# Kernel optimization log

Measured on AMD Instinct MI355X. Metric: run time of the kernel, lower is better.

## Reference

```python
import jax, jax.numpy as jnp
import numpy as np

N, E, IN_F, OUT_F, HEADS = 50000, 800000, 256, 64, 8


def setup_inputs() -> dict:
    key = jax.random.key(0)
    k1, k2, k3, k4, k5 = jax.random.split(key, 5)
    stdv = 1.0 / np.sqrt(OUT_F)
    return {
        "h": jax.random.normal(k1, (N, IN_F), dtype=jnp.float32),
        "weight": jax.random.uniform(k2, (IN_F, OUT_F), minval=-stdv, maxval=stdv, dtype=jnp.float32),
        "attention_w": jax.random.normal(k3, (1, HEADS), dtype=jnp.float32),
        "src": jax.random.randint(k4, (E,), 0, N, dtype=jnp.int32),
        "dst": jax.random.randint(k5, (E,), 0, N, dtype=jnp.int32),
    }


def reference(h, weight, attention_w, src, dst):
    n_nodes = h.shape[0]
    hp = h @ weight                              # [N, F] projected features
    hs = hp[src]                                 # [E, F] gather source feats
    hd = hp[dst]                                 # [E, F] gather dest feats
    dot = jnp.sum(hs * hd, axis=-1, keepdims=True)   # [E, 1] edge dot attention
    # original: (msg[:, F, 1] @ attention_w[1, H]).sum(H) == msg * attention_w.sum()
    msg = dot * hs * jnp.sum(attention_w)        # [E, F]
    accum = jax.ops.segment_sum(msg, dst, num_segments=n_nodes)  # [N, F]
    # DGL update_all: zero in-degree nodes keep their projected feature
    deg = jax.ops.segment_sum(jnp.ones((src.shape[0], 1), hp.dtype), dst, num_segments=n_nodes)
    return jnp.where(deg > 0, accum, hp)
```

## Files before the change

kernel.cpp:

```cpp
#include <hip/hip_runtime.h>

#define IN_F 256
#define OUT_F 64
#define NBKT_MAX 1024
#define PART_BLOCKS 128
#define HIST_BLOCKS 256

typedef __attribute__((ext_vector_type(8))) short short8;
typedef __attribute__((ext_vector_type(4))) float f32x4;
typedef unsigned int uint32;

#define AS_I(f) __builtin_bit_cast(int, f)
#define AS_F(i) __builtin_bit_cast(float, i)
#define DPP_ADD(v, ctrl, rmask) \
    v += AS_F(__builtin_amdgcn_update_dpp(0, AS_I(v), ctrl, rmask, 0xf, true))

__device__ __forceinline__ float half_sum_sel(float p, bool hi) {
    DPP_ADD(p, 0x111, 0xf);
    DPP_ADD(p, 0x112, 0xf);
    DPP_ADD(p, 0x114, 0xf);
    DPP_ADD(p, 0x118, 0xf);
    DPP_ADD(p, 0x142, 0xa);
    float dlo = AS_F(__builtin_amdgcn_readlane(AS_I(p), 31));
    float dhi = AS_F(__builtin_amdgcn_readlane(AS_I(p), 63));
    return hi ? dhi : dlo;
}

__device__ __forceinline__ unsigned short f2bf(float f) {
    uint32 u = __builtin_bit_cast(uint32, f);
    u += 0x7fffu + ((u >> 16) & 1u);
    return (unsigned short)(u >> 16);
}
__device__ __forceinline__ float bf2f(unsigned short s) {
    return __builtin_bit_cast(float, (uint32)s << 16);
}

__global__ __launch_bounds__(256) void gemm_hist_kernel(const float* __restrict__ h,
                                                        const float* __restrict__ w,
                                                        unsigned short* __restrict__ hpb,
                                                        int N,
                                                        const int* __restrict__ dst,
                                                        int* __restrict__ bkt_cnt,
                                                        int E, int NB, int ngemm) {
    __shared__ char smem[32768];
    int b = blockIdx.x, t = threadIdx.x;

    if (b >= ngemm) {
        int* lcnt = (int*)smem;
        int hb = b - ngemm;
        for (int i = t; i < NB; i += 256) lcnt[i] = 0;
        __syncthreads();
        for (int e = hb * 256 + t; e < E; e += HIST_BLOCKS * 256)
            atomicAdd(&lcnt[dst[e] >> 6], 1);
        __syncthreads();
        for (int i = t; i < NB; i += 256)
            if (lcnt[i]) atomicAdd(&bkt_cnt[i], lcnt[i]);
        return;
    }

    short8* wfrag = (short8*)smem;
    for (int slot = t; slot < 2048; slot += 256) {
        int kb = slot >> 6, n = slot & 63;
        short8 v;
#pragma unroll
        for (int jj = 0; jj < 8; ++jj)
            v[jj] = (short)f2bf(w[(size_t)(kb * 8 + jj) * OUT_F + n]);
        wfrag[slot] = v;
    }
    __syncthreads();

    int wave = t >> 6, lane = t & 63;
    int n16  = lane & 15, quad = lane >> 4;
    int base = b * 64 + wave * 16;
    int arow_i = base + n16; if (arow_i >= N) arow_i = N - 1;
    const float* arow = h + (size_t)arow_i * IN_F;

    f32x4 acc[4];
#pragma unroll
    for (int ct = 0; ct < 4; ++ct) acc[ct] = (f32x4){0.f, 0.f, 0.f, 0.f};

#pragma unroll
    for (int ks = 0; ks < 8; ++ks) {
        int k0 = ks * 32;
        float4 a0 = *(const float4*)(arow + k0 + quad * 8);
        float4 a1 = *(const float4*)(arow + k0 + quad * 8 + 4);
        short8 af;
        af[0] = (short)f2bf(a0.x); af[1] = (short)f2bf(a0.y);
        af[2] = (short)f2bf(a0.z); af[3] = (short)f2bf(a0.w);
        af[4] = (short)f2bf(a1.x); af[5] = (short)f2bf(a1.y);
        af[6] = (short)f2bf(a1.z); af[7] = (short)f2bf(a1.w);
        int kb = ks * 4 + quad;
#pragma unroll
        for (int ct = 0; ct < 4; ++ct) {
            short8 bf = wfrag[kb * 64 + ct * 16 + n16];
            acc[ct] = __builtin_amdgcn_mfma_f32_16x16x32_bf16(af, bf, acc[ct], 0, 0, 0);
        }
    }

#pragma unroll
    for (int ct = 0; ct < 4; ++ct) {
#pragma unroll
        for (int r = 0; r < 4; ++r) {
            int ro = base + quad * 4 + r;
            if (ro < N) hpb[(size_t)ro * OUT_F + ct * 16 + n16] = f2bf(acc[ct][r]);
        }
    }
}

__global__ __launch_bounds__(256) void partition_kernel(const int* __restrict__ src,
                                                        const int* __restrict__ dst,
                                                        const int* __restrict__ bkt_cnt,
                                                        int* __restrict__ bkt_cursor,
                                                        int* __restrict__ bkt_base,
                                                        uint32* __restrict__ pairs,
                                                        int E, int NB) {
    __shared__ int sbase[NBKT_MAX + 1];
    __shared__ int lcnt[NBKT_MAX];
    __shared__ int gbase[NBKT_MAX];
    __shared__ int wsum2[4];

    int t = threadIdx.x, lane = t & 63, wid = t >> 6;

    int loc[4];
    int s = 0;
#pragma unroll
    for (int j = 0; j < 4; ++j) {
        int idx = t * 4 + j;
        int x = (idx < NB) ? bkt_cnt[idx] : 0;
        loc[j] = s; s += x;
    }
    int xs = s;
#pragma unroll
    for (int off = 1; off < 64; off <<= 1) {
        int y = __shfl_up(xs, off, 64);
        if (lane >= off) xs += y;
    }
    if (lane == 63) wsum2[wid] = xs;
    __syncthreads();
    int base_w = 0;
    for (int k = 0; k < wid; ++k) base_w += wsum2[k];
    int toff = base_w + xs - s;
#pragma unroll
    for (int j = 0; j < 4; ++j) {
        int idx = t * 4 + j;
        if (idx < NB) sbase[idx] = toff + loc[j];
    }
    if (t == 0) sbase[NB] = E;
    __syncthreads();

    if (blockIdx.x == 0) {
        for (int i = t; i <= NB; i += 256) bkt_base[i] = sbase[i];
    }

    int chunk = (E + PART_BLOCKS - 1) / PART_BLOCKS;
    int s0 = blockIdx.x * chunk;
    int s1 = min(E, s0 + chunk);

    for (int i = t; i < NB; i += 256) lcnt[i] = 0;
    __syncthreads();
    for (int e = s0 + t; e < s1; e += 256)
        atomicAdd(&lcnt[dst[e] >> 6], 1);
    __syncthreads();
    for (int i = t; i < NB; i += 256) {
        int c = lcnt[i];
        if (c) gbase[i] = sbase[i] + atomicAdd(&bkt_cursor[i], c);
        lcnt[i] = 0;
    }
    __syncthreads();
    for (int e = s0 + t; e < s1; e += 256) {
        int d  = dst[e];
        int bk = d >> 6;
        int idx = atomicAdd(&lcnt[bk], 1);
        pairs[gbase[bk] + idx] = (uint32)src[e] | ((uint32)(d & 63) << 26);
    }
}

__global__ __launch_bounds__(256) void sortlocal_kernel(const uint32* __restrict__ pairs,
                                                        const int* __restrict__ bkt_base,
                                                        int* __restrict__ srcs,
                                                        int* __restrict__ row_ptr,
                                                        int N, int E) {
    __shared__ int bin[64], excl[65], cur[64];
    int b = blockIdx.x, t = threadIdx.x;
    int beg = bkt_base[b], end = bkt_base[b + 1];

    if (t < 64) bin[t] = 0;
    __syncthreads();
    for (int i = beg + t; i < end; i += 256)
        atomicAdd(&bin[pairs[i] >> 26], 1);
    __syncthreads();
    if (t < 64) {
        int v = bin[t], x = v;
#pragma unroll
        for (int off = 1; off < 64; off <<= 1) {
            int y = __shfl_up(x, off, 64);
            if (t >= off) x += y;
        }
        excl[t] = x - v;
        cur[t]  = x - v;
        if (t == 63) excl[64] = x;
    }
    __syncthreads();
    if (t < 65) {
        int idx = b * 64 + t;
        if (idx <= N) row_ptr[idx] = beg + excl[t];
    }
    for (int i = beg + t; i < end; i += 256) {
        uint32 p = pairs[i];
        int dl   = (int)(p >> 26);
        int pos  = atomicAdd(&cur[dl], 1);
        srcs[beg + pos] = (int)(p & 0x3FFFFFFu);
    }
}

#define GATH(S) (*(const uint32*)(hpb + (size_t)(S) * OUT_F + half * 2))
#define PROC(Q) { float a0 = bf2f((unsigned short)((Q) & 0xffff));            \
                  float a1 = bf2f((unsigned short)((Q) >> 16));               \
                  float dd = half_sum_sel(fmaf(a1, hd1, a0 * hd0), hi);       \
                  acc0 = fmaf(dd, a0, acc0); acc1 = fmaf(dd, a1, acc1); }

__global__ __launch_bounds__(256) void accum_kernel(const unsigned short* __restrict__ hpb,
                                                    const int* __restrict__ row_ptr,
                                                    const int* __restrict__ srcs,
                                                    const float* __restrict__ attw,
                                                    float* __restrict__ out, int N) {
    int v    = (blockIdx.x * blockDim.x + threadIdx.x) >> 6;
    int lane = threadIdx.x & 63;
    if (v >= N) return;

    int  half = lane & 31;
    bool hi   = lane >= 32;

    int beg = row_ptr[v];
    int end = row_ptr[v + 1];

    uint32 hd2 = *(const uint32*)(hpb + (size_t)v * OUT_F + half * 2);
    float hd0 = bf2f((unsigned short)(hd2 & 0xffff));
    float hd1 = bf2f((unsigned short)(hd2 >> 16));

    float c = 0.f;
#pragma unroll
    for (int i = 0; i < 8; ++i) c += attw[i];

    float acc0 = 0.f, acc1 = 0.f;
    int j = beg;

    for (; j + 32 <= end; j += 32) {
        const int4* sp = (const int4*)(srcs + j);
        int4 sa = sp[0], sb = sp[1], sc = sp[2], sd = sp[3];
        int4 se = sp[4], sf = sp[5], sg = sp[6], sh = sp[7];
        uint32 q0  = GATH(hi ? sa.y : sa.x), q1  = GATH(hi ? sa.w : sa.z);
        uint32 q2  = GATH(hi ? sb.y : sb.x), q3  = GATH(hi ? sb.w : sb.z);
        uint32 q4  = GATH(hi ? sc.y : sc.x), q5  = GATH(hi ? sc.w : sc.z);
        uint32 q6  = GATH(hi ? sd.y : sd.x), q7  = GATH(hi ? sd.w : sd.z);
        uint32 q8  = GATH(hi ? se.y : se.x), q9  = GATH(hi ? se.w : se.z);
        uint32 q10 = GATH(hi ? sf.y : sf.x), q11 = GATH(hi ? sf.w : sf.z);
        uint32 q12 = GATH(hi ? sg.y : sg.x), q13 = GATH(hi ? sg.w : sg.z);
        uint32 q14 = GATH(hi ? sh.y : sh.x), q15 = GATH(hi ? sh.w : sh.z);
        PROC(q0)  PROC(q1)  PROC(q2)  PROC(q3)
        PROC(q4)  PROC(q5)  PROC(q6)  PROC(q7)
        PROC(q8)  PROC(q9)  PROC(q10) PROC(q11)
        PROC(q12) PROC(q13) PROC(q14) PROC(q15)
    }
    for (; j + 8 <= end; j += 8) {
        const int4* sp = (const int4*)(srcs + j);
        int4 sa = sp[0], sb = sp[1];
        uint32 q0 = GATH(hi ? sa.y : sa.x), q1 = GATH(hi ? sa.w : sa.z);
        uint32 q2 = GATH(hi ? sb.y : sb.x), q3 = GATH(hi ? sb.w : sb.z);
        PROC(q0) PROC(q1) PROC(q2) PROC(q3)
    }
    for (; j + 2 <= end; j += 2) {
        int s_lo = srcs[j], s_hi = srcs[j + 1];
        uint32 q = GATH(hi ? s_hi : s_lo);
        PROC(q)
    }
    if (j < end) {
        uint32 q = GATH(srcs[j]);
        float a0 = bf2f((unsigned short)(q & 0xffff));
        float a1 = bf2f((unsigned short)(q >> 16));
        float dd = half_sum_sel(fmaf(a1, hd1, a0 * hd0), false);
        if (!hi) {
            acc0 = fmaf(dd, a0, acc0);
            acc1 = fmaf(dd, a1, acc1);
        }
    }

    acc0 += __shfl_xor(acc0, 32, 64);
    acc1 += __shfl_xor(acc1, 32, 64);

    if (!hi) {
        float r0, r1;
        if (end > beg) { r0 = acc0 * c; r1 = acc1 * c; }
        else           { r0 = hd0;      r1 = hd1;      }
        *(float2*)(out + (size_t)v * OUT_F + half * 2) = make_float2(r0, r1);
    }
}

extern "C" void kernel_launch(void* const* d_in, const int* in_sizes, int n_in,
                              void* d_out, int out_size, void* d_ws, size_t ws_size,
                              hipStream_t stream) {
    const float* h    = (const float*)d_in[0];
    const float* w    = (const float*)d_in[1];
    const float* attw = (const float*)d_in[2];
    const int*   src  = (const int*)d_in[3];
    const int*   dst  = (const int*)d_in[4];

    int N = in_sizes[0] / IN_F;
    int E = in_sizes[3];
    int NB = (N + 63) >> 6;
    int ngemm = (N + 63) / 64;

    float* out = (float*)d_out;

    char* p = (char*)d_ws;
    unsigned short* hpb = (unsigned short*)p;  p += (size_t)N * OUT_F * sizeof(unsigned short);
    int* bkt_cnt    = (int*)p;                 p += (NBKT_MAX + 1) * sizeof(int);
    int* bkt_cursor = (int*)p;                 p += (NBKT_MAX + 1) * sizeof(int);
    int* bkt_base   = (int*)p;                 p += (NBKT_MAX + 1) * sizeof(int);
    int* row_ptr    = (int*)p;                 p += ((size_t)N + 8) * sizeof(int);
    uint32* pairs   = (uint32*)p;              p += (size_t)E * sizeof(uint32);
    int* srcs       = (int*)p;

    hipMemsetAsync(bkt_cnt, 0, 2 * (NBKT_MAX + 1) * sizeof(int), stream);

    gemm_hist_kernel<<<ngemm + HIST_BLOCKS, 256, 0, stream>>>(h, w, hpb, N,
                                                              dst, bkt_cnt, E, NB, ngemm);

    partition_kernel<<<PART_BLOCKS, 256, 0, stream>>>(src, dst, bkt_cnt, bkt_cursor,
                                                      bkt_base, pairs, E, NB);

    sortlocal_kernel<<<NB, 256, 0, stream>>>(pairs, bkt_base, srcs, row_ptr, N, E);

    accum_kernel<<<((size_t)N * 64 + 255) / 256, 256, 0, stream>>>(hpb, row_ptr, srcs, attw, out, N);
}
```

Measured before the change: 172.5 us.

## Fuse bucket-local sort into accumulation kernel using LDS-resident source lists

Removes the separate sortlocal kernel and its srcs/row_ptr global arrays. Each 512-thread block now sorts its 64-node bucket's pairs into shared memory and then aggregates all 64 nodes from LDS, with 8 waves each handling 8 nodes. This saves one kernel launch and a global write/read round trip of the edge list. Buckets larger than CAP fall back to a slow linear scan. The partition kernel moves to 512 threads, and the accumulation inner unroll shrinks from 32 to 16 edges.

```diff
diff --git a/kernel.cpp b/kernel.cpp
--- a/kernel.cpp
+++ b/kernel.cpp
@@ -5,6 +5,7 @@
 #define NBKT_MAX 1024
 #define PART_BLOCKS 128
 #define HIST_BLOCKS 256
+#define CAP 3072
 
 typedef __attribute__((ext_vector_type(8))) short short8;
 typedef __attribute__((ext_vector_type(4))) float f32x4;
@@ -107,7 +108,7 @@
     }
 }
 
-__global__ __launch_bounds__(256) void partition_kernel(const int* __restrict__ src,
+__global__ __launch_bounds__(512) void partition_kernel(const int* __restrict__ src,
                                                         const int* __restrict__ dst,
                                                         const int* __restrict__ bkt_cnt,
                                                         int* __restrict__ bkt_cursor,
@@ -117,18 +118,15 @@
     __shared__ int sbase[NBKT_MAX + 1];
     __shared__ int lcnt[NBKT_MAX];
     __shared__ int gbase[NBKT_MAX];
-    __shared__ int wsum2[4];
+    __shared__ int wsum2[8];
 
     int t = threadIdx.x, lane = t & 63, wid = t >> 6;
 
-    int loc[4];
-    int s = 0;
-#pragma unroll
-    for (int j = 0; j < 4; ++j) {
-        int idx = t * 4 + j;
-        int x = (idx < NB) ? bkt_cnt[idx] : 0;
-        loc[j] = s; s += x;
-    }
+    int loc0, loc1;
+    int x0 = (t * 2     < NB) ? bkt_cnt[t * 2]     : 0;
+    int x1 = (t * 2 + 1 < NB) ? bkt_cnt[t * 2 + 1] : 0;
+    loc0 = 0; loc1 = x0;
+    int s = x0 + x1;
     int xs = s;
 #pragma unroll
     for (int off = 1; off < 64; off <<= 1) {
@@ -140,76 +138,35 @@
     int base_w = 0;
     for (int k = 0; k < wid; ++k) base_w += wsum2[k];
     int toff = base_w + xs - s;
-#pragma unroll
-    for (int j = 0; j < 4; ++j) {
-        int idx = t * 4 + j;
-        if (idx < NB) sbase[idx] = toff + loc[j];
-    }
+    if (t * 2     < NB) sbase[t * 2]     = toff + loc0;
+    if (t * 2 + 1 < NB) sbase[t * 2 + 1] = toff + loc1;
     if (t == 0) sbase[NB] = E;
     __syncthreads();
 
     if (blockIdx.x == 0) {
-        for (int i = t; i <= NB; i += 256) bkt_base[i] = sbase[i];
+        for (int i = t; i <= NB; i += 512) bkt_base[i] = sbase[i];
     }
 
     int chunk = (E + PART_BLOCKS - 1) / PART_BLOCKS;
     int s0 = blockIdx.x * chunk;
     int s1 = min(E, s0 + chunk);
 
-    for (int i = t; i < NB; i += 256) lcnt[i] = 0;
-    __syncthreads();
-    for (int e = s0 + t; e < s1; e += 256)
+    for (int i = t; i < NB; i += 512) lcnt[i] = 0;
+    __syncthreads();
+    for (int e = s0 + t; e < s1; e += 512)
         atomicAdd(&lcnt[dst[e] >> 6], 1);
     __syncthreads();
-    for (int i = t; i < NB; i += 256) {
+    for (int i = t; i < NB; i += 512) {
         int c = lcnt[i];
         if (c) gbase[i] = sbase[i] + atomicAdd(&bkt_cursor[i], c);
         lcnt[i] = 0;
     }
     __syncthreads();
-    for (int e = s0 + t; e < s1; e += 256) {
+    for (int e = s0 + t; e < s1; e += 512) {
         int d  = dst[e];
         int bk = d >> 6;
         int idx = atomicAdd(&lcnt[bk], 1);
         pairs[gbase[bk] + idx] = (uint32)src[e] | ((uint32)(d & 63) << 26);
-    }
-}
-
-__global__ __launch_bounds__(256) void sortlocal_kernel(const uint32* __restrict__ pairs,
-                                                        const int* __restrict__ bkt_base,
-                                                        int* __restrict__ srcs,
-                                                        int* __restrict__ row_ptr,
-                                                        int N, int E) {
-    __shared__ int bin[64], excl[65], cur[64];
-    int b = blockIdx.x, t = threadIdx.x;
-    int beg = bkt_base[b], end = bkt_base[b + 1];
-
-    if (t < 64) bin[t] = 0;
-    __syncthreads();
-    for (int i = beg + t; i < end; i += 256)
-        atomicAdd(&bin[pairs[i] >> 26], 1);
-    __syncthreads();
-    if (t < 64) {
-        int v = bin[t], x = v;
-#pragma unroll
-        for (int off = 1; off < 64; off <<= 1) {
-            int y = __shfl_up(x, off, 64);
-            if (t >= off) x += y;
-        }
-        excl[t] = x - v;
-        cur[t]  = x - v;
-        if (t == 63) excl[64] = x;
-    }
-    __syncthreads();
-    if (t < 65) {
-        int idx = b * 64 + t;
-        if (idx <= N) row_ptr[idx] = beg + excl[t];
-    }
-    for (int i = beg + t; i < end; i += 256) {
-        uint32 p = pairs[i];
-        int dl   = (int)(p >> 26);
-        int pos  = atomicAdd(&cur[dl], 1);
-        srcs[beg + pos] = (int)(p & 0x3FFFFFFu);
     }
 }
 
@@ -219,80 +176,148 @@
                   float dd = half_sum_sel(fmaf(a1, hd1, a0 * hd0), hi);       \
                   acc0 = fmaf(dd, a0, acc0); acc1 = fmaf(dd, a1, acc1); }
 
-__global__ __launch_bounds__(256) void accum_kernel(const unsigned short* __restrict__ hpb,
-                                                    const int* __restrict__ row_ptr,
-                                                    const int* __restrict__ srcs,
-                                                    const float* __restrict__ attw,
-                                                    float* __restrict__ out, int N) {
-    int v    = (blockIdx.x * blockDim.x + threadIdx.x) >> 6;
-    int lane = threadIdx.x & 63;
-    if (v >= N) return;
-
-    int  half = lane & 31;
-    bool hi   = lane >= 32;
-
-    int beg = row_ptr[v];
-    int end = row_ptr[v + 1];
-
-    uint32 hd2 = *(const uint32*)(hpb + (size_t)v * OUT_F + half * 2);
-    float hd0 = bf2f((unsigned short)(hd2 & 0xffff));
-    float hd1 = bf2f((unsigned short)(hd2 >> 16));
+__global__ __launch_bounds__(512) void accum_sort_kernel(const unsigned short* __restrict__ hpb,
+                                                         const uint32* __restrict__ pairs,
+                                                         const int* __restrict__ bkt_base,
+                                                         const float* __restrict__ attw,
+                                                         float* __restrict__ out, int N) {
+    __shared__ int slds[CAP];
+    __shared__ int bin[64], excl[65], cur[64];
+
+    int b = blockIdx.x, t = threadIdx.x;
+    int wid = t >> 6, lane = t & 63;
+    int half = lane & 31;
+    bool hi  = lane >= 32;
+    int node0 = b * 64;
+
+    int beg = bkt_base[b], end = bkt_base[b + 1];
+    int nE  = end - beg;
 
     float c = 0.f;
 #pragma unroll
     for (int i = 0; i < 8; ++i) c += attw[i];
 
-    float acc0 = 0.f, acc1 = 0.f;
-    int j = beg;
-
-    for (; j + 32 <= end; j += 32) {
-        const int4* sp = (const int4*)(srcs + j);
-        int4 sa = sp[0], sb = sp[1], sc = sp[2], sd = sp[3];
-        int4 se = sp[4], sf = sp[5], sg = sp[6], sh = sp[7];
-        uint32 q0  = GATH(hi ? sa.y : sa.x), q1  = GATH(hi ? sa.w : sa.z);
-        uint32 q2  = GATH(hi ? sb.y : sb.x), q3  = GATH(hi ? sb.w : sb.z);
-        uint32 q4  = GATH(hi ? sc.y : sc.x), q5  = GATH(hi ? sc.w : sc.z);
-        uint32 q6  = GATH(hi ? sd.y : sd.x), q7  = GATH(hi ? sd.w : sd.z);
-        uint32 q8  = GATH(hi ? se.y : se.x), q9  = GATH(hi ? se.w : se.z);
-        uint32 q10 = GATH(hi ? sf.y : sf.x), q11 = GATH(hi ? sf.w : sf.z);
-        uint32 q12 = GATH(hi ? sg.y : sg.x), q13 = GATH(hi ? sg.w : sg.z);
-        uint32 q14 = GATH(hi ? sh.y : sh.x), q15 = GATH(hi ? sh.w : sh.z);
-        PROC(q0)  PROC(q1)  PROC(q2)  PROC(q3)
-        PROC(q4)  PROC(q5)  PROC(q6)  PROC(q7)
-        PROC(q8)  PROC(q9)  PROC(q10) PROC(q11)
-        PROC(q12) PROC(q13) PROC(q14) PROC(q15)
-    }
-    for (; j + 8 <= end; j += 8) {
-        const int4* sp = (const int4*)(srcs + j);
-        int4 sa = sp[0], sb = sp[1];
-        uint32 q0 = GATH(hi ? sa.y : sa.x), q1 = GATH(hi ? sa.w : sa.z);
-        uint32 q2 = GATH(hi ? sb.y : sb.x), q3 = GATH(hi ? sb.w : sb.z);
-        PROC(q0) PROC(q1) PROC(q2) PROC(q3)
-    }
-    for (; j + 2 <= end; j += 2) {
-        int s_lo = srcs[j], s_hi = srcs[j + 1];
-        uint32 q = GATH(hi ? s_hi : s_lo);
-        PROC(q)
-    }
-    if (j < end) {
-        uint32 q = GATH(srcs[j]);
-        float a0 = bf2f((unsigned short)(q & 0xffff));
-        float a1 = bf2f((unsigned short)(q >> 16));
-        float dd = half_sum_sel(fmaf(a1, hd1, a0 * hd0), false);
-        if (!hi) {
-            acc0 = fmaf(dd, a0, acc0);
-            acc1 = fmaf(dd, a1, acc1);
-        }
-    }
-
-    acc0 += __shfl_xor(acc0, 32, 64);
-    acc1 += __shfl_xor(acc1, 32, 64);
-
-    if (!hi) {
-        float r0, r1;
-        if (end > beg) { r0 = acc0 * c; r1 = acc1 * c; }
-        else           { r0 = hd0;      r1 = hd1;      }
-        *(float2*)(out + (size_t)v * OUT_F + half * 2) = make_float2(r0, r1);
+    if (nE <= CAP) {
+        if (t < 64) bin[t] = 0;
+        __syncthreads();
+        for (int i = beg + t; i < end; i += 512)
+            atomicAdd(&bin[pairs[i] >> 26], 1);
+        __syncthreads();
+        if (t < 64) {
+            int v = bin[t], x = v;
+#pragma unroll
+            for (int off = 1; off < 64; off <<= 1) {
+                int y = __shfl_up(x, off, 64);
+                if (t >= off) x += y;
+            }
+            excl[t] = x - v;
+            cur[t]  = x - v;
+            if (t == 63) excl[64] = x;
+        }
+        __syncthreads();
+        for (int i = beg + t; i < end; i += 512) {
+            uint32 p = pairs[i];
+            int dl   = (int)(p >> 26);
+            int pos  = atomicAdd(&cur[dl], 1);
+            slds[pos] = (int)(p & 0x3FFFFFFu);
+        }
+        __syncthreads();
+
+#pragma unroll 1
+        for (int k = 0; k < 8; ++k) {
+            int n    = wid + 8 * k;
+            int node = node0 + n;
+            if (node >= N) continue;
+
+            int jb = excl[n], je = excl[n + 1];
+
+            uint32 hd2 = *(const uint32*)(hpb + (size_t)node * OUT_F + half * 2);
+            float hd0 = bf2f((unsigned short)(hd2 & 0xffff));
+            float hd1 = bf2f((unsigned short)(hd2 >> 16));
+
+            float acc0 = 0.f, acc1 = 0.f;
+            int j = jb;
+            int sel = hi ? 1 : 0;
+
+            for (; j + 16 <= je; j += 16) {
+                int i0 = slds[j + 0  + sel], i1 = slds[j + 2  + sel];
+                int i2 = slds[j + 4  + sel], i3 = slds[j + 6  + sel];
+                int i4 = slds[j + 8  + sel], i5 = slds[j + 10 + sel];
+                int i6 = slds[j + 12 + sel], i7 = slds[j + 14 + sel];
+                uint32 q0 = GATH(i0), q1 = GATH(i1), q2 = GATH(i2), q3 = GATH(i3);
+                uint32 q4 = GATH(i4), q5 = GATH(i5), q6 = GATH(i6), q7 = GATH(i7);
+                PROC(q0) PROC(q1) PROC(q2) PROC(q3)
+                PROC(q4) PROC(q5) PROC(q6) PROC(q7)
+            }
+            for (; j + 8 <= je; j += 8) {
+                int i0 = slds[j + 0 + sel], i1 = slds[j + 2 + sel];
+                int i2 = slds[j + 4 + sel], i3 = slds[j + 6 + sel];
+                uint32 q0 = GATH(i0), q1 = GATH(i1), q2 = GATH(i2), q3 = GATH(i3);
+                PROC(q0) PROC(q1) PROC(q2) PROC(q3)
+            }
+            for (; j + 2 <= je; j += 2) {
+                int i0 = slds[j + sel];
+                uint32 q0 = GATH(i0);
+                PROC(q0)
+            }
+            if (j < je) {
+                int i0 = slds[j];
+                uint32 q0 = GATH(i0);
+                float a0 = bf2f((unsigned short)(q0 & 0xffff));
+                float a1 = bf2f((unsigned short)(q0 >> 16));
+                float dd = half_sum_sel(fmaf(a1, hd1, a0 * hd0), false);
+                if (!hi) {
+                    acc0 = fmaf(dd, a0, acc0);
+                    acc1 = fmaf(dd, a1, acc1);
+                }
+            }
+
+            acc0 += __shfl_xor(acc0, 32, 64);
+            acc1 += __shfl_xor(acc1, 32, 64);
+
+            if (!hi) {
+                float r0, r1;
+                if (je > jb) { r0 = acc0 * c; r1 = acc1 * c; }
+                else         { r0 = hd0;      r1 = hd1;      }
+                *(float2*)(out + (size_t)node * OUT_F + half * 2) = make_float2(r0, r1);
+            }
+        }
+    } else {
+#pragma unroll 1
+        for (int k = 0; k < 8; ++k) {
+            int n    = wid + 8 * k;
+            int node = node0 + n;
+            if (node >= N) continue;
+
+            uint32 hd2 = *(const uint32*)(hpb + (size_t)node * OUT_F + half * 2);
+            float hd0 = bf2f((unsigned short)(hd2 & 0xffff));
+            float hd1 = bf2f((unsigned short)(hd2 >> 16));
+
+            float acc0 = 0.f, acc1 = 0.f;
+            int deg = 0;
+            for (int i = beg; i < end; ++i) {
+                uint32 p = pairs[i];
+                if ((int)(p >> 26) == n) {
+                    ++deg;
+                    uint32 q0 = GATH((int)(p & 0x3FFFFFFu));
+                    float a0 = bf2f((unsigned short)(q0 & 0xffff));
+                    float a1 = bf2f((unsigned short)(q0 >> 16));
+                    float dd = half_sum_sel(fmaf(a1, hd1, a0 * hd0), false);
+                    if (!hi) {
+                        acc0 = fmaf(dd, a0, acc0);
+                        acc1 = fmaf(dd, a1, acc1);
+                    }
+                }
+            }
+            acc0 += __shfl_xor(acc0, 32, 64);
+            acc1 += __shfl_xor(acc1, 32, 64);
+            if (!hi) {
+                float r0, r1;
+                if (deg > 0) { r0 = acc0 * c; r1 = acc1 * c; }
+                else         { r0 = hd0;      r1 = hd1;      }
+                *(float2*)(out + (size_t)node * OUT_F + half * 2) = make_float2(r0, r1);
+            }
+        }
     }
 }
 
@@ -317,19 +342,15 @@
     int* bkt_cnt    = (int*)p;                 p += (NBKT_MAX + 1) * sizeof(int);
     int* bkt_cursor = (int*)p;                 p += (NBKT_MAX + 1) * sizeof(int);
     int* bkt_base   = (int*)p;                 p += (NBKT_MAX + 1) * sizeof(int);
-    int* row_ptr    = (int*)p;                 p += ((size_t)N + 8) * sizeof(int);
-    uint32* pairs   = (uint32*)p;              p += (size_t)E * sizeof(uint32);
-    int* srcs       = (int*)p;
+    uint32* pairs   = (uint32*)p;
 
     hipMemsetAsync(bkt_cnt, 0, 2 * (NBKT_MAX + 1) * sizeof(int), stream);
 
     gemm_hist_kernel<<<ngemm + HIST_BLOCKS, 256, 0, stream>>>(h, w, hpb, N,
                                                               dst, bkt_cnt, E, NB, ngemm);
 
-    partition_kernel<<<PART_BLOCKS, 256, 0, stream>>>(src, dst, bkt_cnt, bkt_cursor,
+    partition_kernel<<<PART_BLOCKS, 512, 0, stream>>>(src, dst, bkt_cnt, bkt_cursor,
                                                       bkt_base, pairs, E, NB);
 
-    sortlocal_kernel<<<NB, 256, 0, stream>>>(pairs, bkt_base, srcs, row_ptr, N, E);
-
-    accum_kernel<<<((size_t)N * 64 + 255) / 256, 256, 0, stream>>>(hpb, row_ptr, srcs, attw, out, N);
-}
+    accum_sort_kernel<<<NB, 512, 0, stream>>>(hpb, pairs, bkt_base, attw, out, N);
+}
```

Result: faster. 154.8 us (-10.3%).
